# Kernel optimization log

Measured on AMD Instinct MI355X. Metric: run time of the kernel, lower is better.

Reference implementation:

```python
import jax, jax.numpy as jnp
import numpy as np

K = 3  # number of propagation hops (matches init kwarg)
N = 50000
E = 800000
D = 96


def setup_inputs() -> dict:
    key = jax.random.key(0)
    k1, k2, k3, k4 = jax.random.split(key, 4)
    x = jax.random.normal(k1, (N, D), dtype=jnp.float32)
    edge_feature = jax.random.normal(k2, (E, D), dtype=jnp.float32)
    hopwise = jnp.ones((K + 1,), dtype=jnp.float32)  # nn.Parameter(torch.ones(K+1))
    edge_index = jax.random.randint(k3, (2, E), 0, N, dtype=jnp.int64)
    return {"x": x, "edge_feature": edge_feature, "hopwise": hopwise,
            "edge_index": edge_index}


def reference(x, edge_feature, hopwise, edge_index):
    row, col = edge_index[0], edge_index[1]
    n = x.shape[0]
    # degree of destination nodes (col), symmetric normalization
    deg = jax.ops.segment_sum(jnp.ones(col.shape, x.dtype), col, num_segments=n)
    deg_inv = jnp.where(deg > 0, jax.lax.rsqrt(jnp.maximum(deg, 1.0)) * jnp.where(deg > 0, 1.0, 0.0), 0.0)
    deg_inv = jnp.where(deg > 0, deg ** -0.5, 0.0)
    norm = (deg_inv[row] * deg_inv[col])[:, None]  # [E, 1]
    hidden = x * hopwise[0]
    for hop in range(K):
        # message: norm * (x_j + edge_feature); aggregate: scatter-add at col
        msg = norm * (x[row] + edge_feature)          # [E, D]
        x = jax.ops.segment_sum(msg, col, num_segments=n)  # [N, D]
        hidden = hidden + hopwise[hop + 1] * x
    return hidden
```

## Files before the change

### kernel.cpp

```cpp
#include <hip/hip_runtime.h>


__global__ void deg_kernel(const int* __restrict__ col, int* __restrict__ deg, int E) {
    int e = blockIdx.x * blockDim.x + threadIdx.x;
    if (e < E) atomicAdd(&deg[col[e]], 1);
}

__global__ void deginv_kernel(const int* __restrict__ deg, float* __restrict__ deginv, int n) {
    int i = blockIdx.x * blockDim.x + threadIdx.x;
    if (i < n) {
        int d = deg[i];
        deginv[i] = (d > 0) ? rsqrtf((float)d) : 0.0f;
    }
}

__global__ __launch_bounds__(256) void scan1_kernel(const int* __restrict__ deg,
                                                    int* __restrict__ starts,
                                                    int* __restrict__ bsums, int n) {
    int t = threadIdx.x;
    int i = blockIdx.x * 1024 + t * 4;
    int4 v = make_int4(0, 0, 0, 0);
    if (i + 3 < n) v = *(const int4*)(deg + i);
    else {
        if (i + 0 < n) v.x = deg[i + 0];
        if (i + 1 < n) v.y = deg[i + 1];
        if (i + 2 < n) v.z = deg[i + 2];
        if (i + 3 < n) v.w = deg[i + 3];
    }
    int s0 = v.x, s1 = s0 + v.y, s2 = s1 + v.z, s3 = s2 + v.w;
    int tot = s3;
    int lane = t & 63;
    int incl = tot;
    for (int off = 1; off < 64; off <<= 1) {
        int u = __shfl_up(incl, off, 64);
        if (lane >= off) incl += u;
    }
    __shared__ int wsum[4];
    __shared__ int woff[4];
    int wid = t >> 6;
    if (lane == 63) wsum[wid] = incl;
    __syncthreads();
    if (t == 0) { int a = 0; for (int w = 0; w < 4; ++w) { woff[w] = a; a += wsum[w]; } }
    __syncthreads();
    int excl = incl - tot + woff[wid];
    if (i + 0 < n) starts[i + 0] = excl;
    if (i + 1 < n) starts[i + 1] = excl + s0;
    if (i + 2 < n) starts[i + 2] = excl + s1;
    if (i + 3 < n) starts[i + 3] = excl + s2;
    if (t == 255) bsums[blockIdx.x] = woff[3] + wsum[3];
}

__global__ __launch_bounds__(64) void scan2_kernel(int* __restrict__ bsums, int nb,
                                                   int* __restrict__ starts, int n, int total) {
    int lane = threadIdx.x;
    int v = (lane < nb) ? bsums[lane] : 0;
    int incl = v;
    for (int off = 1; off < 64; off <<= 1) {
        int u = __shfl_up(incl, off, 64);
        if (lane >= off) incl += u;
    }
    if (lane < nb) bsums[lane] = incl - v;
    if (lane == 0) starts[n] = total;
}

__global__ __launch_bounds__(256) void scan3_kernel(int* __restrict__ starts,
                                                    int* __restrict__ cursor,
                                                    const int* __restrict__ bsums, int n) {
    int t = threadIdx.x;
    int i = blockIdx.x * 1024 + t * 4;
    int off = bsums[blockIdx.x];
    for (int k = 0; k < 4; ++k) {
        int ii = i + k;
        if (ii < n) {
            int s = starts[ii] + off;
            starts[ii] = s;
            cursor[ii] = s;
        }
    }
}

__global__ void fill_kernel(const int* __restrict__ col, int* __restrict__ cursor,
                            int* __restrict__ eids, int E) {
    int e = blockIdx.x * blockDim.x + threadIdx.x;
    if (e < E) {
        int pos = atomicAdd(&cursor[col[e]], 1);
        eids[pos] = e;
    }
}

__global__ void slot_kernel(const int* __restrict__ eids, const int* __restrict__ row,
                            const int* __restrict__ col, const float* __restrict__ deginv,
                            float2* __restrict__ edat, int E) {
    int j = blockIdx.x * blockDim.x + threadIdx.x;
    if (j < E) {
        int e = eids[j];
        int r = row[e], c = col[e];
        float2 o;
        o.x = __int_as_float(r);
        o.y = deginv[r] * deginv[c];
        edat[j] = o;
    }
}

__global__ __launch_bounds__(96) void b_kernel(const int* __restrict__ starts,
                                               const int* __restrict__ eids,
                                               const float2* __restrict__ edat,
                                               const float* __restrict__ ef,
                                               float* __restrict__ bvec, int D) {
    int node = blockIdx.x;
    int d = threadIdx.x;
    int s = starts[node], e_end = starts[node + 1];
    float acc = 0.0f;
    int j = s;
    for (; j + 4 <= e_end; j += 4) {
        int e0 = eids[j], e1 = eids[j + 1], e2 = eids[j + 2], e3 = eids[j + 3];
        float n0 = edat[j].y, n1 = edat[j + 1].y, n2 = edat[j + 2].y, n3 = edat[j + 3].y;
        float f0 = ef[(size_t)e0 * D + d];
        float f1 = ef[(size_t)e1 * D + d];
        float f2 = ef[(size_t)e2 * D + d];
        float f3 = ef[(size_t)e3 * D + d];
        acc += n0 * f0 + n1 * f1 + n2 * f2 + n3 * f3;
    }
    for (; j < e_end; ++j) {
        acc += edat[j].y * ef[(size_t)eids[j] * D + d];
    }
    bvec[(size_t)node * D + d] = acc;
}

__global__ void init_out_kernel(const float* __restrict__ x, const float* __restrict__ hopwise,
                                float* __restrict__ out, int n4) {
    int i = blockIdx.x * blockDim.x + threadIdx.x;
    if (i < n4) {
        float h0 = hopwise[0];
        float4 v = ((const float4*)x)[i];
        float4 o;
        o.x = h0 * v.x; o.y = h0 * v.y; o.z = h0 * v.z; o.w = h0 * v.w;
        ((float4*)out)[i] = o;
    }
}

__global__ __launch_bounds__(96) void hop_kernel(const int* __restrict__ starts,
                                                 const float2* __restrict__ edat,
                                                 const float* __restrict__ xcur,
                                                 const float* __restrict__ bvec,
                                                 float* __restrict__ xnext,
                                                 float* __restrict__ out,
                                                 const float* __restrict__ hopwise,
                                                 int hop, int D) {
    int node = blockIdx.x;
    int d = threadIdx.x;
    int s = starts[node], e_end = starts[node + 1];
    float acc = 0.0f;
    int j = s;
    for (; j + 4 <= e_end; j += 4) {
        float2 a0 = edat[j], a1 = edat[j + 1], a2 = edat[j + 2], a3 = edat[j + 3];
        int r0 = __float_as_int(a0.x), r1 = __float_as_int(a1.x);
        int r2 = __float_as_int(a2.x), r3 = __float_as_int(a3.x);
        float x0 = xcur[(size_t)r0 * D + d];
        float x1 = xcur[(size_t)r1 * D + d];
        float x2 = xcur[(size_t)r2 * D + d];
        float x3 = xcur[(size_t)r3 * D + d];
        acc += a0.y * x0 + a1.y * x1 + a2.y * x2 + a3.y * x3;
    }
    for (; j < e_end; ++j) {
        float2 a = edat[j];
        acc += a.y * xcur[(size_t)__float_as_int(a.x) * D + d];
    }
    size_t o = (size_t)node * D + d;
    float xv = acc + bvec[o];
    xnext[o] = xv;
    out[o] += hopwise[hop] * xv;
}

extern "C" void kernel_launch(void* const* d_in, const int* in_sizes, int n_in,
                              void* d_out, int out_size, void* d_ws, size_t ws_size,
                              hipStream_t stream) {
    const float* x       = (const float*)d_in[0];
    const float* ef      = (const float*)d_in[1];
    const float* hopwise = (const float*)d_in[2];
    const int*   eidx    = (const int*)d_in[3];

    const int E = in_sizes[3] / 2;
    const int D = in_sizes[1] / E;
    const int N = in_sizes[0] / D;
    const int K = in_sizes[2] - 1;
    const int ND4 = (N * D) / 4;

    const int* row = eidx;
    const int* col = eidx + E;
    float* out = (float*)d_out;

    char* w = (char*)d_ws;
    int*    deg    = (int*)w;     w += (size_t)N * 4;
    int*    starts = (int*)w;     w += (size_t)(N + 8) * 4;
    int*    cursor = (int*)w;     w += (size_t)N * 4;
    int*    eids   = (int*)w;     w += (size_t)E * 4;
    float*  deginv = (float*)w;   w += (size_t)N * 4;
    int*    bsums  = (int*)w;     w += 256 * 4;
    float2* edat   = (float2*)w;  w += (size_t)E * 8;
    float*  bvec   = (float*)w;   w += (size_t)N * D * 4;
    float*  buf0   = (float*)w;   w += (size_t)N * D * 4;
    float*  buf1   = (float*)w;

    const int BT = 256;
    const int nScanBlocks = (N + 1023) / 1024;

    hipMemsetAsync(deg, 0, (size_t)N * sizeof(int), stream);
    deg_kernel<<<(E + BT - 1) / BT, BT, 0, stream>>>(col, deg, E);
    deginv_kernel<<<(N + BT - 1) / BT, BT, 0, stream>>>(deg, deginv, N);
    scan1_kernel<<<nScanBlocks, 256, 0, stream>>>(deg, starts, bsums, N);
    scan2_kernel<<<1, 64, 0, stream>>>(bsums, nScanBlocks, starts, N, E);
    scan3_kernel<<<nScanBlocks, 256, 0, stream>>>(starts, cursor, bsums, N);
    fill_kernel<<<(E + BT - 1) / BT, BT, 0, stream>>>(col, cursor, eids, E);
    slot_kernel<<<(E + BT - 1) / BT, BT, 0, stream>>>(eids, row, col, deginv, edat, E);

    b_kernel<<<N, D, 0, stream>>>(starts, eids, edat, ef, bvec, D);

    init_out_kernel<<<(ND4 + BT - 1) / BT, BT, 0, stream>>>(x, hopwise, out, ND4);

    const float* xcur = x;
    for (int hop = 0; hop < K; ++hop) {
        float* xnext = (hop & 1) ? buf1 : buf0;
        hop_kernel<<<N, D, 0, stream>>>(starts, edat, xcur, bvec, xnext, out,
                                        hopwise, hop + 1, D);
        xcur = xnext;
    }
}
```

Measured before the change: 734.4 us.

## Fuse bias, init and first hop; vectorize hops with float4 chunk threads

Merges the edge-feature bias kernel, the output init kernel and the first propagation hop into one kernel that gathers both edge features and source node features per edge. All hop kernels now assign one thread per 4-float chunk of a node (24 chunks per node, 256-thread blocks) and use float4 loads instead of one block of 96 threads per node. This removes two launches and one full pass over out and bvec, and widens the memory transactions. In exchange each thread carries more registers, and per-node work is no longer aligned to block boundaries.

Measured after the change: 687.3 us. -6.4%, faster.

```diff
diff --git a/kernel.cpp b/kernel.cpp
--- a/kernel.cpp
+++ b/kernel.cpp
@@ -102,74 +102,110 @@
     }
 }
 
-__global__ __launch_bounds__(96) void b_kernel(const int* __restrict__ starts,
-                                               const int* __restrict__ eids,
-                                               const float2* __restrict__ edat,
-                                               const float* __restrict__ ef,
-                                               float* __restrict__ bvec, int D) {
-    int node = blockIdx.x;
-    int d = threadIdx.x;
+#define CH 24
+
+__global__ __launch_bounds__(256) void hop1_kernel(const int* __restrict__ starts,
+                                                   const float2* __restrict__ edat,
+                                                   const int* __restrict__ eids,
+                                                   const float4* __restrict__ ef4,
+                                                   const float4* __restrict__ x4,
+                                                   float4* __restrict__ bvec4,
+                                                   float4* __restrict__ xnext4,
+                                                   float4* __restrict__ out4,
+                                                   const float* __restrict__ hopwise,
+                                                   int NC) {
+    int g = blockIdx.x * 256 + threadIdx.x;
+    if (g >= NC) return;
+    int node = g / CH;
+    int c = g - node * CH;
     int s = starts[node], e_end = starts[node + 1];
-    float acc = 0.0f;
+    float4 ab = make_float4(0.f, 0.f, 0.f, 0.f);
+    float4 ax = make_float4(0.f, 0.f, 0.f, 0.f);
     int j = s;
-    for (; j + 4 <= e_end; j += 4) {
-        int e0 = eids[j], e1 = eids[j + 1], e2 = eids[j + 2], e3 = eids[j + 3];
-        float n0 = edat[j].y, n1 = edat[j + 1].y, n2 = edat[j + 2].y, n3 = edat[j + 3].y;
-        float f0 = ef[(size_t)e0 * D + d];
-        float f1 = ef[(size_t)e1 * D + d];
-        float f2 = ef[(size_t)e2 * D + d];
-        float f3 = ef[(size_t)e3 * D + d];
-        acc += n0 * f0 + n1 * f1 + n2 * f2 + n3 * f3;
+    for (; j + 2 <= e_end; j += 2) {
+        float2 a0 = edat[j], a1 = edat[j + 1];
+        int e0 = eids[j], e1 = eids[j + 1];
+        int r0 = __float_as_int(a0.x), r1 = __float_as_int(a1.x);
+        float4 f0 = ef4[(size_t)e0 * CH + c];
+        float4 f1 = ef4[(size_t)e1 * CH + c];
+        float4 v0 = x4[(size_t)r0 * CH + c];
+        float4 v1 = x4[(size_t)r1 * CH + c];
+        ab.x += a0.y * f0.x + a1.y * f1.x;
+        ab.y += a0.y * f0.y + a1.y * f1.y;
+        ab.z += a0.y * f0.z + a1.y * f1.z;
+        ab.w += a0.y * f0.w + a1.y * f1.w;
+        ax.x += a0.y * v0.x + a1.y * v1.x;
+        ax.y += a0.y * v0.y + a1.y * v1.y;
+        ax.z += a0.y * v0.z + a1.y * v1.z;
+        ax.w += a0.y * v0.w + a1.y * v1.w;
     }
     for (; j < e_end; ++j) {
-        acc += edat[j].y * ef[(size_t)eids[j] * D + d];
-    }
-    bvec[(size_t)node * D + d] = acc;
-}
-
-__global__ void init_out_kernel(const float* __restrict__ x, const float* __restrict__ hopwise,
-                                float* __restrict__ out, int n4) {
-    int i = blockIdx.x * blockDim.x + threadIdx.x;
-    if (i < n4) {
-        float h0 = hopwise[0];
-        float4 v = ((const float4*)x)[i];
-        float4 o;
-        o.x = h0 * v.x; o.y = h0 * v.y; o.z = h0 * v.z; o.w = h0 * v.w;
-        ((float4*)out)[i] = o;
-    }
-}
-
-__global__ __launch_bounds__(96) void hop_kernel(const int* __restrict__ starts,
-                                                 const float2* __restrict__ edat,
-                                                 const float* __restrict__ xcur,
-                                                 const float* __restrict__ bvec,
-                                                 float* __restrict__ xnext,
-                                                 float* __restrict__ out,
-                                                 const float* __restrict__ hopwise,
-                                                 int hop, int D) {
-    int node = blockIdx.x;
-    int d = threadIdx.x;
+        float2 a = edat[j];
+        int e = eids[j];
+        int r = __float_as_int(a.x);
+        float4 f = ef4[(size_t)e * CH + c];
+        float4 v = x4[(size_t)r * CH + c];
+        ab.x += a.y * f.x; ab.y += a.y * f.y; ab.z += a.y * f.z; ab.w += a.y * f.w;
+        ax.x += a.y * v.x; ax.y += a.y * v.y; ax.z += a.y * v.z; ax.w += a.y * v.w;
+    }
+    float h0 = hopwise[0], h1 = hopwise[1];
+    size_t o = (size_t)node * CH + c;
+    float4 xself = x4[o];
+    float4 x1;
+    x1.x = ax.x + ab.x; x1.y = ax.y + ab.y; x1.z = ax.z + ab.z; x1.w = ax.w + ab.w;
+    bvec4[o] = ab;
+    xnext4[o] = x1;
+    float4 ov;
+    ov.x = h0 * xself.x + h1 * x1.x;
+    ov.y = h0 * xself.y + h1 * x1.y;
+    ov.z = h0 * xself.z + h1 * x1.z;
+    ov.w = h0 * xself.w + h1 * x1.w;
+    out4[o] = ov;
+}
+
+__global__ __launch_bounds__(256) void hop_kernel(const int* __restrict__ starts,
+                                                  const float2* __restrict__ edat,
+                                                  const float4* __restrict__ xcur4,
+                                                  const float4* __restrict__ bvec4,
+                                                  float4* __restrict__ xnext4,
+                                                  float4* __restrict__ out4,
+                                                  const float* __restrict__ hopwise,
+                                                  int hop, int NC) {
+    int g = blockIdx.x * 256 + threadIdx.x;
+    if (g >= NC) return;
+    int node = g / CH;
+    int c = g - node * CH;
     int s = starts[node], e_end = starts[node + 1];
-    float acc = 0.0f;
+    float4 ax = make_float4(0.f, 0.f, 0.f, 0.f);
     int j = s;
     for (; j + 4 <= e_end; j += 4) {
         float2 a0 = edat[j], a1 = edat[j + 1], a2 = edat[j + 2], a3 = edat[j + 3];
         int r0 = __float_as_int(a0.x), r1 = __float_as_int(a1.x);
         int r2 = __float_as_int(a2.x), r3 = __float_as_int(a3.x);
-        float x0 = xcur[(size_t)r0 * D + d];
-        float x1 = xcur[(size_t)r1 * D + d];
-        float x2 = xcur[(size_t)r2 * D + d];
-        float x3 = xcur[(size_t)r3 * D + d];
-        acc += a0.y * x0 + a1.y * x1 + a2.y * x2 + a3.y * x3;
+        float4 v0 = xcur4[(size_t)r0 * CH + c];
+        float4 v1 = xcur4[(size_t)r1 * CH + c];
+        float4 v2 = xcur4[(size_t)r2 * CH + c];
+        float4 v3 = xcur4[(size_t)r3 * CH + c];
+        ax.x += a0.y * v0.x + a1.y * v1.x + a2.y * v2.x + a3.y * v3.x;
+        ax.y += a0.y * v0.y + a1.y * v1.y + a2.y * v2.y + a3.y * v3.y;
+        ax.z += a0.y * v0.z + a1.y * v1.z + a2.y * v2.z + a3.y * v3.z;
+        ax.w += a0.y * v0.w + a1.y * v1.w + a2.y * v2.w + a3.y * v3.w;
     }
     for (; j < e_end; ++j) {
         float2 a = edat[j];
-        acc += a.y * xcur[(size_t)__float_as_int(a.x) * D + d];
-    }
-    size_t o = (size_t)node * D + d;
-    float xv = acc + bvec[o];
-    xnext[o] = xv;
-    out[o] += hopwise[hop] * xv;
+        int r = __float_as_int(a.x);
+        float4 v = xcur4[(size_t)r * CH + c];
+        ax.x += a.y * v.x; ax.y += a.y * v.y; ax.z += a.y * v.z; ax.w += a.y * v.w;
+    }
+    float h = hopwise[hop];
+    size_t o = (size_t)node * CH + c;
+    float4 b = bvec4[o];
+    float4 xv;
+    xv.x = ax.x + b.x; xv.y = ax.y + b.y; xv.z = ax.z + b.z; xv.w = ax.w + b.w;
+    xnext4[o] = xv;
+    float4 ov = out4[o];
+    ov.x += h * xv.x; ov.y += h * xv.y; ov.z += h * xv.z; ov.w += h * xv.w;
+    out4[o] = ov;
 }
 
 extern "C" void kernel_launch(void* const* d_in, const int* in_sizes, int n_in,
@@ -184,7 +220,7 @@
     const int D = in_sizes[1] / E;
     const int N = in_sizes[0] / D;
     const int K = in_sizes[2] - 1;
-    const int ND4 = (N * D) / 4;
+    const int NC = N * (D / 4);
 
     const int* row = eidx;
     const int* col = eidx + E;
@@ -214,15 +250,18 @@
     fill_kernel<<<(E + BT - 1) / BT, BT, 0, stream>>>(col, cursor, eids, E);
     slot_kernel<<<(E + BT - 1) / BT, BT, 0, stream>>>(eids, row, col, deginv, edat, E);
 
-    b_kernel<<<N, D, 0, stream>>>(starts, eids, edat, ef, bvec, D);
-
-    init_out_kernel<<<(ND4 + BT - 1) / BT, BT, 0, stream>>>(x, hopwise, out, ND4);
-
-    const float* xcur = x;
-    for (int hop = 0; hop < K; ++hop) {
+    int hopBlocks = (NC + 255) / 256;
+    hop1_kernel<<<hopBlocks, 256, 0, stream>>>(starts, edat, eids, (const float4*)ef,
+                                               (const float4*)x, (float4*)bvec,
+                                               (float4*)buf0, (float4*)out, hopwise, NC);
+
+    const float* xcur = buf0;
+    for (int hop = 2; hop <= K; ++hop) {
         float* xnext = (hop & 1) ? buf1 : buf0;
-        hop_kernel<<<N, D, 0, stream>>>(starts, edat, xcur, bvec, xnext, out,
-                                        hopwise, hop + 1, D);
+        if (xnext == xcur) xnext = (xcur == buf0) ? buf1 : buf0;
+        hop_kernel<<<hopBlocks, 256, 0, stream>>>(starts, edat, (const float4*)xcur,
+                                                  (const float4*)bvec, (float4*)xnext,
+                                                  (float4*)out, hopwise, hop, NC);
         xcur = xnext;
     }
 }
```
